# Kernel tuning notes

Hardware: AMD Instinct MI355X
Metric: run time of the kernel (lower is better)

The kernel has to match this reference:

```python
import jax, jax.numpy as jnp
import numpy as np

B, N, M, L, H = 32, 4096, 256, 128, 4
GAMMA = 2.0


def setup_inputs() -> dict:
    key = jax.random.key(0)
    kx, km, kv, ku, kw = jax.random.split(key, 5)
    x = jax.random.normal(kx, (B, N, M), dtype=jnp.float32)
    masks = (jax.random.uniform(km, (B, N)) > 0.3).astype(jnp.float32)
    # VarianceScaling(scale=0.1, fan_in, uniform) ~ small init; exact dist doesn't affect math
    V = jax.random.normal(kv, (H, M, L), dtype=jnp.float32) * 0.02
    U = jax.random.normal(ku, (H, M, L), dtype=jnp.float32) * 0.02
    w = jax.random.normal(kw, (H, L, 1), dtype=jnp.float32) * 0.05
    return {"x": x, "masks": masks, "V": V, "U": U, "w": w}


def reference(x, masks, V, U, w):
    # x: [B,N,M], masks: [B,N], V/U: [H,M,L], w: [H,L,1]
    m = masks[:, None, :, None]  # [B,1,N,1] broadcast over heads
    gated = jnp.tanh(jnp.einsum('bnm,hml->bhnl', x, V)) * jax.nn.sigmoid(
        jnp.einsum('bnm,hml->bhnl', x, U))          # [B,H,N,L]
    logits = jnp.einsum('bhnl,hl->bhn', gated, w[..., 0])[..., None]  # [B,H,N,1]
    a = m * logits                                   # masked logits (as in original)
    a = m * jnp.exp(a)                               # masked exp
    a = a / jnp.sum(a, axis=2, keepdims=True)        # softmax over instances
    ag = a ** GAMMA
    a = ag / jnp.sum(ag, axis=2, keepdims=True)      # gamma-power renorm
    emb = jnp.einsum('bhnk,bnm->bhm', a, x)          # weighted sum; k is the trailing 1
    emb = emb.reshape(B, H * M)                      # concat heads along axis=1
    att = jnp.transpose(a, (1, 0, 2, 3))             # [H,B,N,1] (per-head attention list)
    return (att, emb)
```

## Files before the change

kernel.cpp:

```cpp
#include <hip/hip_runtime.h>
#include <hip/hip_bf16.h>
#include <stdint.h>

#define B_ 32
#define N_ 4096
#define M_ 256
#define L_ 128
#define H_ 4
#define BN_ (B_ * N_)

typedef __bf16 bf16x8 __attribute__((ext_vector_type(8)));
typedef float  f32x4  __attribute__((ext_vector_type(4)));

__device__ __forceinline__ unsigned short f2bf(float f) {
    unsigned int u = __float_as_uint(f);
    u += 0x7fffu + ((u >> 16) & 1u);
    return (unsigned short)(u >> 16);
}
__device__ __forceinline__ unsigned int pack2(float lo, float hi) {
    return (unsigned int)f2bf(lo) | ((unsigned int)f2bf(hi) << 16);
}

__device__ __forceinline__ void gload16(const void* g, void* l) {
    __builtin_amdgcn_global_load_lds(
        (const __attribute__((address_space(1))) unsigned int*)g,
        (__attribute__((address_space(3))) unsigned int*)l, 16, 0, 0);
}


__global__ void prep_x(const float* __restrict__ x, unsigned short* __restrict__ xb) {
    const int blk  = blockIdx.x;
    const int tile = blk >> 2, ks = blk & 3;
    const int i    = threadIdx.x;
    const int kk   = (i & 7) * 8;
    const int tl   = kk >> 5;
    const int kl   = kk & 31;
    char* dst = (char*)xb + ((size_t)tile * 8 + ks * 2 + tl) * 8192;
#pragma unroll
    for (int rep = 0; rep < 4; ++rep) {
        int row = rep * 32 + (i >> 3);
        const float* gx = x + (size_t)(tile * 128 + row) * M_ + ks * 64 + kk;
        float4 a = *(const float4*)gx;
        float4 b = *(const float4*)(gx + 4);
        uint4 o;
        o.x = pack2(a.x, a.y); o.y = pack2(a.z, a.w);
        o.z = pack2(b.x, b.y); o.w = pack2(b.z, b.w);
        int byte = (row * 64 + kl * 2) ^ ((row & 14) << 3);
        *(uint4*)(dst + byte) = o;
    }
}

__global__ void prep_vu_img(const float* __restrict__ V, const float* __restrict__ U,
                            unsigned short* __restrict__ vu) {
    __shared__ float slab[64][129];
    const int b   = blockIdx.x;
    const int mat = b & 1, ks = (b >> 1) & 3, h = b >> 3;
    const float* src = (mat ? U : V) + ((size_t)h * M_ + ks * 64) * L_;
    const int tid = threadIdx.x;
#pragma unroll
    for (int rep = 0; rep < 32; ++rep) {
        int idx = rep * 256 + tid;
        slab[idx >> 7][idx & 127] = src[(size_t)(idx >> 7) * L_ + (idx & 127)];
    }
    __syncthreads();
#pragma unroll
    for (int rep = 0; rep < 4; ++rep) {
        int cidx = rep * 256 + tid;
        int l  = cidx >> 3;
        int kk = (cidx & 7) * 8;
        uint4 o;
        o.x = pack2(slab[kk + 0][l], slab[kk + 1][l]);
        o.y = pack2(slab[kk + 2][l], slab[kk + 3][l]);
        o.z = pack2(slab[kk + 4][l], slab[kk + 5][l]);
        o.w = pack2(slab[kk + 6][l], slab[kk + 7][l]);
        int tl = kk >> 5, kl = kk & 31;
        char* dst = (char*)vu + (((size_t)(h * 8 + ks * 2 + tl)) * 2 + mat) * 8192;
        int byte = (l * 64 + kl * 2) ^ ((l & 14) << 3);
        *(uint4*)(dst + byte) = o;
    }
}

__global__ __launch_bounds__(256, 3)
void gemm_fast6(const unsigned short* __restrict__ xb,
                const unsigned short* __restrict__ vu,
                const float* __restrict__ w,
                float* __restrict__ logits) {
    __shared__ __align__(16) unsigned short xs[2][4096];
    __shared__ __align__(16) unsigned short vs[2][4096];
    __shared__ __align__(16) unsigned short us[2][4096];
    __shared__ float part[2][128];

    const int orig    = blockIdx.x;
    const int logical = (orig & 7) * 512 + (orig >> 3);
    const int tile    = logical >> 2;
    const int h       = logical & 3;

    const int tid  = threadIdx.x;
    const int lane = tid & 63;
    const int wv   = tid >> 6;
    const int g    = lane >> 4;
    const int c    = lane & 15;
    const int wr   = wv & 1;
    const int wc   = wv >> 1;

    f32x4 accV[4][4], accU[4][4];
#pragma unroll
    for (int rf = 0; rf < 4; ++rf)
#pragma unroll
        for (int cf = 0; cf < 4; ++cf) {
            accV[rf][cf] = (f32x4){0.f, 0.f, 0.f, 0.f};
            accU[rf][cf] = (f32x4){0.f, 0.f, 0.f, 0.f};
        }

    const int soff = wv * 2048;

    const char* gxs = (const char*)xb + (size_t)tile * 65536 + soff + lane * 16;
    const char* gvs = (const char*)vu + (size_t)h * 131072 + soff + lane * 16;
    const char* gus = gvs + 8192;

    int aoff[4], boff[4];
#pragma unroll
    for (int rf = 0; rf < 4; ++rf) {
        int r = wr * 64 + rf * 16 + c;
        aoff[rf] = (r * 64 + g * 16) ^ ((r & 14) << 3);
    }
#pragma unroll
    for (int cf = 0; cf < 4; ++cf) {
        int l = wc * 64 + cf * 16 + c;
        boff[cf] = (l * 64 + g * 16) ^ ((l & 14) << 3);
    }

#define SCHED __builtin_amdgcn_sched_barrier(0)

#define STAGE(t, bufi) do {                                          \
        const char* _gx = gxs + (t) * 8192;                          \
        const char* _gv = gvs + (t) * 16384;                         \
        const char* _gu = gus + (t) * 16384;                         \
        gload16(_gx,        (char*)xs[bufi] + soff);                 \
        gload16(_gx + 1024, (char*)xs[bufi] + soff + 1024);          \
        gload16(_gv,        (char*)vs[bufi] + soff);                 \
        gload16(_gv + 1024, (char*)vs[bufi] + soff + 1024);          \
        gload16(_gu,        (char*)us[bufi] + soff);                 \
        gload16(_gu + 1024, (char*)us[bufi] + soff + 1024);          \
    } while (0)

    STAGE(0, 0);
    SCHED;

#pragma unroll
    for (int t = 0; t < 8; ++t) {
        asm volatile("s_waitcnt vmcnt(0)" ::: "memory");
        __builtin_amdgcn_s_barrier();
        SCHED;

        if (t < 7) STAGE(t + 1, (t + 1) & 1);
        SCHED;

        const int buf = t & 1;
        const char* xbuf = (const char*)xs[buf];
        const char* vbuf = (const char*)vs[buf];
        const char* ubuf = (const char*)us[buf];

        bf16x8 a0 = *(const bf16x8*)(xbuf + aoff[0]);
        bf16x8 a1 = *(const bf16x8*)(xbuf + aoff[1]);
        bf16x8 a2 = *(const bf16x8*)(xbuf + aoff[2]);
        bf16x8 a3 = *(const bf16x8*)(xbuf + aoff[3]);
        __builtin_amdgcn_s_setprio(1);
#pragma unroll
        for (int cf = 0; cf < 4; ++cf) {
            bf16x8 bv = *(const bf16x8*)(vbuf + boff[cf]);
            bf16x8 bu = *(const bf16x8*)(ubuf + boff[cf]);
            accV[0][cf] = __builtin_amdgcn_mfma_f32_16x16x32_bf16(a0, bv, accV[0][cf], 0, 0, 0);
            accV[1][cf] = __builtin_amdgcn_mfma_f32_16x16x32_bf16(a1, bv, accV[1][cf], 0, 0, 0);
            accV[2][cf] = __builtin_amdgcn_mfma_f32_16x16x32_bf16(a2, bv, accV[2][cf], 0, 0, 0);
            accV[3][cf] = __builtin_amdgcn_mfma_f32_16x16x32_bf16(a3, bv, accV[3][cf], 0, 0, 0);
            accU[0][cf] = __builtin_amdgcn_mfma_f32_16x16x32_bf16(a0, bu, accU[0][cf], 0, 0, 0);
            accU[1][cf] = __builtin_amdgcn_mfma_f32_16x16x32_bf16(a1, bu, accU[1][cf], 0, 0, 0);
            accU[2][cf] = __builtin_amdgcn_mfma_f32_16x16x32_bf16(a2, bu, accU[2][cf], 0, 0, 0);
            accU[3][cf] = __builtin_amdgcn_mfma_f32_16x16x32_bf16(a3, bu, accU[3][cf], 0, 0, 0);
        }
        __builtin_amdgcn_s_setprio(0);
    }
#undef STAGE
#undef SCHED

    const float* wrow = w + h * L_ + wc * 64;
#pragma unroll
    for (int rf = 0; rf < 4; ++rf) {
        float plog[4] = {0.f, 0.f, 0.f, 0.f};
#pragma unroll
        for (int cf = 0; cf < 4; ++cf) {
            float wvv = wrow[cf * 16 + c];
#pragma unroll
            for (int i = 0; i < 4; ++i) {
                float vv = accV[rf][cf][i];
                float uu = accU[rf][cf][i];
                vv = fminf(fmaxf(vv, -20.f), 20.f);
                float A = __expf(2.f * vv);
                float E = __expf(fminf(-uu, 30.f));
                float gg = __fdividef(A - 1.f, (A + 1.f) * (1.f + E));
                plog[i] += gg * wvv;
            }
        }
#pragma unroll
        for (int i = 0; i < 4; ++i) {
            float v = plog[i];
            v += __shfl_xor(v, 1);
            v += __shfl_xor(v, 2);
            v += __shfl_xor(v, 4);
            v += __shfl_xor(v, 8);
            if (c == 0)
                part[wc][wr * 64 + rf * 16 + g * 4 + i] = v;
        }
    }
    __syncthreads();
    if (tid < 128) {
        float v = part[0][tid] + part[1][tid];
        int rowflat = tile * 128 + tid;
        int b = rowflat >> 12;
        int n = rowflat & (N_ - 1);
        logits[((size_t)b * H_ + h) * N_ + n] = v;
    }
}

__global__ void prep_vu_slow(const float* __restrict__ V, const float* __restrict__ U,
                             unsigned short* __restrict__ Vt, unsigned short* __restrict__ Ut) {
    int idx = blockIdx.x * 256 + threadIdx.x;
    int m = idx & (M_ - 1);
    int l = (idx >> 8) & (L_ - 1);
    int h = idx >> 15;
    Vt[idx] = f2bf(V[((size_t)h * M_ + m) * L_ + l]);
    Ut[idx] = f2bf(U[((size_t)h * M_ + m) * L_ + l]);
}

#define BM 128
#define BK 64

__global__ __launch_bounds__(256, 2)
void gemm_logits(const float* __restrict__ x,
                 const unsigned short* __restrict__ Vt,
                 const unsigned short* __restrict__ Ut,
                 const float* __restrict__ w,
                 float* __restrict__ logits) {
    __shared__ __align__(16) unsigned short xs[BM * BK];
    __shared__ __align__(16) unsigned short vs[L_ * BK];
    __shared__ __align__(16) unsigned short us[L_ * BK];
    __shared__ float wl[L_];

    const int h    = blockIdx.x >> 10;
    const int tile = blockIdx.x & 1023;
    const int row0 = tile * BM;
    const int tid  = threadIdx.x;
    const int lane = tid & 63;
    const int wave = tid >> 6;

    if (tid < L_) wl[tid] = w[h * L_ + tid];

    f32x4 accV[2][8], accU[2][8];
#pragma unroll
    for (int rf = 0; rf < 2; ++rf)
#pragma unroll
        for (int cf = 0; cf < 8; ++cf) {
            accV[rf][cf] = (f32x4){0.f, 0.f, 0.f, 0.f};
            accU[rf][cf] = (f32x4){0.f, 0.f, 0.f, 0.f};
        }

    const unsigned short* Vh = Vt + (size_t)h * L_ * M_;
    const unsigned short* Uh = Ut + (size_t)h * L_ * M_;
    const int g = lane >> 4;
    const int c = lane & 15;

    for (int ks = 0; ks < 4; ++ks) {
        const int k0 = ks * BK;
        __syncthreads();
#pragma unroll
        for (int p = 0; p < 4; ++p) {
            int row = p * 32 + (tid >> 3);
            int kk  = (tid & 7) * 8;
            const float* gx = x + (size_t)(row0 + row) * M_ + k0 + kk;
            float4 a = *(const float4*)gx;
            float4 b = *(const float4*)(gx + 4);
            uint4 o;
            o.x = pack2(a.x, a.y); o.y = pack2(a.z, a.w);
            o.z = pack2(b.x, b.y); o.w = pack2(b.z, b.w);
            int byte = (row * BK + kk) * 2;
            byte ^= (row & 7) << 4;
            *(uint4*)((char*)xs + byte) = o;
        }
#pragma unroll
        for (int p = 0; p < 4; ++p) {
            int l  = p * 32 + (tid >> 3);
            int kk = (tid & 7) * 8;
            uint4 v = *(const uint4*)(Vh + (size_t)l * M_ + k0 + kk);
            uint4 u = *(const uint4*)(Uh + (size_t)l * M_ + k0 + kk);
            int byte = (l * BK + kk) * 2;
            byte ^= (l & 7) << 4;
            *(uint4*)((char*)vs + byte) = v;
            *(uint4*)((char*)us + byte) = u;
        }
        __syncthreads();
#pragma unroll
        for (int ksub = 0; ksub < 2; ++ksub) {
            bf16x8 afr[2];
#pragma unroll
            for (int rf = 0; rf < 2; ++rf) {
                int row = wave * 32 + rf * 16 + c;
                int byte = (row * BK + ksub * 32 + g * 8) * 2;
                byte ^= (row & 7) << 4;
                afr[rf] = *(const bf16x8*)((const char*)xs + byte);
            }
#pragma unroll
            for (int cf = 0; cf < 8; ++cf) {
                int l = cf * 16 + c;
                int byte = (l * BK + ksub * 32 + g * 8) * 2;
                byte ^= (l & 7) << 4;
                bf16x8 bv = *(const bf16x8*)((const char*)vs + byte);
                bf16x8 bu = *(const bf16x8*)((const char*)us + byte);
#pragma unroll
                for (int rf = 0; rf < 2; ++rf) {
                    accV[rf][cf] = __builtin_amdgcn_mfma_f32_16x16x32_bf16(afr[rf], bv, accV[rf][cf], 0, 0, 0);
                    accU[rf][cf] = __builtin_amdgcn_mfma_f32_16x16x32_bf16(afr[rf], bu, accU[rf][cf], 0, 0, 0);
                }
            }
        }
    }
#pragma unroll
    for (int rf = 0; rf < 2; ++rf) {
        float plog[4] = {0.f, 0.f, 0.f, 0.f};
#pragma unroll
        for (int cf = 0; cf < 8; ++cf) {
            float wvv = wl[cf * 16 + c];
#pragma unroll
            for (int i = 0; i < 4; ++i) {
                float vv = accV[rf][cf][i];
                float uu = accU[rf][cf][i];
                vv = fminf(fmaxf(vv, -20.f), 20.f);
                float e2v = __expf(2.f * vv);
                float t = __fdividef(e2v - 1.f, e2v + 1.f);
                float s = __fdividef(1.f, 1.f + __expf(-uu));
                plog[i] += t * s * wvv;
            }
        }
#pragma unroll
        for (int i = 0; i < 4; ++i) {
            float v = plog[i];
            v += __shfl_xor(v, 1);
            v += __shfl_xor(v, 2);
            v += __shfl_xor(v, 4);
            v += __shfl_xor(v, 8);
            if (c == 0) {
                int rowflat = row0 + wave * 32 + rf * 16 + g * 4 + i;
                int b = rowflat >> 12;
                int n = rowflat & (N_ - 1);
                logits[((size_t)b * H_ + h) * N_ + n] = v;
            }
        }
    }
}

__global__ __launch_bounds__(256)
void softmax_att(const float* __restrict__ logits, const float* __restrict__ masks,
                 float* __restrict__ att) {
    const int bh = blockIdx.x;
    const int b = bh >> 2, h = bh & 3;
    __shared__ float e2s[N_];
    __shared__ float red[4];
    const int tid = threadIdx.x;

    float sum = 0.f;
#pragma unroll
    for (int i = 0; i < N_ / 256; ++i) {
        int n = i * 256 + tid;
        float lg = logits[((size_t)b * H_ + h) * N_ + n];
        float mv = masks[(size_t)b * N_ + n];
        float e = mv * __expf(mv * lg);
        float e2 = e * e;
        e2s[n] = e2;
        sum += e2;
    }
#pragma unroll
    for (int off = 32; off >= 1; off >>= 1) sum += __shfl_xor(sum, off);
    if ((tid & 63) == 0) red[tid >> 6] = sum;
    __syncthreads();
    float S = red[0] + red[1] + red[2] + red[3];
    float inv = 1.f / S;
#pragma unroll
    for (int i = 0; i < N_ / 256; ++i) {
        int n = i * 256 + tid;
        att[((size_t)h * B_ + b) * N_ + n] = e2s[n] * inv;
    }
}

#define NCH 32
#define CHUNK (N_ / NCH)

__global__ __launch_bounds__(256)
void emb_partial(const float* __restrict__ x, const float* __restrict__ att,
                 float* __restrict__ part) {
    const int bc = blockIdx.x;
    const int b = bc >> 5, ch = bc & 31;
    __shared__ float as[H_][CHUNK];
    const int tid = threadIdx.x;

    for (int i = tid; i < H_ * CHUNK; i += 256) {
        int hh = i >> 7;
        int j  = i & (CHUNK - 1);
        as[hh][j] = att[((size_t)hh * B_ + b) * N_ + ch * CHUNK + j];
    }
    __syncthreads();

    float a0 = 0.f, a1 = 0.f, a2 = 0.f, a3 = 0.f;
    const float* xp = x + ((size_t)b * N_ + ch * CHUNK) * M_ + tid;
#pragma unroll 4
    for (int j = 0; j < CHUNK; ++j) {
        float xv = xp[(size_t)j * M_];
        a0 += as[0][j] * xv;
        a1 += as[1][j] * xv;
        a2 += as[2][j] * xv;
        a3 += as[3][j] * xv;
    }
    float* pp = part + (size_t)bc * H_ * M_ + tid;
    pp[0 * M_] = a0; pp[1 * M_] = a1; pp[2 * M_] = a2; pp[3 * M_] = a3;
}

__global__ __launch_bounds__(256)
void emb_reduce(const float* __restrict__ part, float* __restrict__ emb) {
    int idx = blockIdx.x * 256 + threadIdx.x;
    int b = idx >> 10;
    int r = idx & 1023;
    float s = 0.f;
#pragma unroll
    for (int ci = 0; ci < NCH; ++ci)
        s += part[((size_t)(b * NCH + ci)) * (H_ * M_) + r];
    emb[idx] = s;
}

extern "C" void kernel_launch(void* const* d_in, const int* in_sizes, int n_in,
                              void* d_out, int out_size, void* d_ws, size_t ws_size,
                              hipStream_t stream) {
    const float* x     = (const float*)d_in[0];
    const float* masks = (const float*)d_in[1];
    const float* V     = (const float*)d_in[2];
    const float* U     = (const float*)d_in[3];
    const float* w     = (const float*)d_in[4];

    float* att = (float*)d_out;
    float* emb = att + (size_t)H_ * B_ * N_;

    char* ws = (char*)d_ws;
    const size_t XB_BYTES  = (size_t)1024 * 8 * 8192;
    const size_t VU_BYTES  = (size_t)64 * 8192;
    const size_t LG_BYTES  = (size_t)B_ * H_ * N_ * 4;
    const size_t PT_BYTES  = (size_t)B_ * NCH * H_ * M_ * 4;
    const size_t NEED_FAST = XB_BYTES + VU_BYTES + LG_BYTES + PT_BYTES;

    float* logits;
    float* partp;

    if (ws_size >= NEED_FAST) {
        unsigned short* xb = (unsigned short*)ws;
        unsigned short* vuimg = (unsigned short*)(ws + XB_BYTES);
        logits = (float*)(ws + XB_BYTES + VU_BYTES);
        partp  = (float*)(ws + XB_BYTES + VU_BYTES + LG_BYTES);

        prep_x     <<<4096, 256, 0, stream>>>(x, xb);
        prep_vu_img<<<32,   256, 0, stream>>>(V, U, vuimg);
        gemm_fast6 <<<4096, 256, 0, stream>>>(xb, vuimg, w, logits);
    } else {
        unsigned short* Vt = (unsigned short*)ws;
        unsigned short* Ut = (unsigned short*)(ws + 262144);
        logits = (float*)(ws + 524288);
        partp  = (float*)(ws + 524288 + LG_BYTES);

        prep_vu_slow<<<512, 256, 0, stream>>>(V, U, Vt, Ut);
        gemm_logits <<<4096, 256, 0, stream>>>(x, Vt, Ut, w, logits);
    }

    softmax_att<<<B_ * H_,              256, 0, stream>>>(logits, masks, att);
    emb_partial<<<B_ * NCH,             256, 0, stream>>>(x, att, partp);
    emb_reduce <<<(B_ * H_ * M_) / 256, 256, 0, stream>>>(partp, emb);
}
```

Before: 174.0 us.

## Fuse fp32-to-bf16 x conversion into GEMM and prescale weights for cheaper gating

Removes the separate prep_x pass, which wrote a bf16 swizzled copy of x to a workspace. The GEMM now loads fp32 x straight into registers, converts it in-kernel and writes it to LDS after the MFMA block, overlapping that work with compute. V is prescaled by 2 and U by -1 so the epilogue can call exp directly, dropping the clamps and multiplies. This saves a full write and re-read of x, but adds VALU conversion and register pressure to the GEMM. Without the clamps, exp can overflow to inf and the tanh expression can become NaN for large activations.

```diff
diff --git a/kernel.cpp b/kernel.cpp
--- a/kernel.cpp
+++ b/kernel.cpp
@@ -28,39 +28,18 @@
 }
 
 
-__global__ void prep_x(const float* __restrict__ x, unsigned short* __restrict__ xb) {
-    const int blk  = blockIdx.x;
-    const int tile = blk >> 2, ks = blk & 3;
-    const int i    = threadIdx.x;
-    const int kk   = (i & 7) * 8;
-    const int tl   = kk >> 5;
-    const int kl   = kk & 31;
-    char* dst = (char*)xb + ((size_t)tile * 8 + ks * 2 + tl) * 8192;
-#pragma unroll
-    for (int rep = 0; rep < 4; ++rep) {
-        int row = rep * 32 + (i >> 3);
-        const float* gx = x + (size_t)(tile * 128 + row) * M_ + ks * 64 + kk;
-        float4 a = *(const float4*)gx;
-        float4 b = *(const float4*)(gx + 4);
-        uint4 o;
-        o.x = pack2(a.x, a.y); o.y = pack2(a.z, a.w);
-        o.z = pack2(b.x, b.y); o.w = pack2(b.z, b.w);
-        int byte = (row * 64 + kl * 2) ^ ((row & 14) << 3);
-        *(uint4*)(dst + byte) = o;
-    }
-}
-
 __global__ void prep_vu_img(const float* __restrict__ V, const float* __restrict__ U,
                             unsigned short* __restrict__ vu) {
     __shared__ float slab[64][129];
     const int b   = blockIdx.x;
     const int mat = b & 1, ks = (b >> 1) & 3, h = b >> 3;
     const float* src = (mat ? U : V) + ((size_t)h * M_ + ks * 64) * L_;
+    const float scale = mat ? -1.0f : 2.0f;
     const int tid = threadIdx.x;
 #pragma unroll
     for (int rep = 0; rep < 32; ++rep) {
         int idx = rep * 256 + tid;
-        slab[idx >> 7][idx & 127] = src[(size_t)(idx >> 7) * L_ + (idx & 127)];
+        slab[idx >> 7][idx & 127] = scale * src[(size_t)(idx >> 7) * L_ + (idx & 127)];
     }
     __syncthreads();
 #pragma unroll
@@ -81,7 +60,7 @@
 }
 
 __global__ __launch_bounds__(256, 3)
-void gemm_fast6(const unsigned short* __restrict__ xb,
+void gemm_fast7(const float* __restrict__ x,
                 const unsigned short* __restrict__ vu,
                 const float* __restrict__ w,
                 float* __restrict__ logits) {
@@ -114,9 +93,15 @@
 
     const int soff = wv * 2048;
 
-    const char* gxs = (const char*)xb + (size_t)tile * 65536 + soff + lane * 16;
     const char* gvs = (const char*)vu + (size_t)h * 131072 + soff + lane * 16;
     const char* gus = gvs + 8192;
+
+    const int rL   = lane >> 1;
+    const int half = lane & 1;
+    const float* gx = x + ((size_t)tile * 128 + wv * 32 + rL) * M_ + half * 16;
+
+    const int xrow = wv * 32 + rL;
+    const int xb0  = (xrow * 64 + half * 32) ^ ((xrow & 14) << 3);
 
     int aoff[4], boff[4];
 #pragma unroll
@@ -130,21 +115,46 @@
         boff[cf] = (l * 64 + g * 16) ^ ((l & 14) << 3);
     }
 
+    float4 xr0, xr1, xr2, xr3;
+
 #define SCHED __builtin_amdgcn_sched_barrier(0)
 
-#define STAGE(t, bufi) do {                                          \
-        const char* _gx = gxs + (t) * 8192;                          \
+#define LOADX(t) do {                                                \
+        xr0 = *(const float4*)(gx + (t) * 32);                       \
+        xr1 = *(const float4*)(gx + (t) * 32 + 4);                   \
+        xr2 = *(const float4*)(gx + (t) * 32 + 8);                   \
+        xr3 = *(const float4*)(gx + (t) * 32 + 12);                  \
+    } while (0)
+
+#define WRITEX(bufi) do {                                            \
+        bf16x8 lo, hi;                                               \
+        lo[0] = (__bf16)xr0.x; lo[1] = (__bf16)xr0.y;                \
+        lo[2] = (__bf16)xr0.z; lo[3] = (__bf16)xr0.w;                \
+        lo[4] = (__bf16)xr1.x; lo[5] = (__bf16)xr1.y;                \
+        lo[6] = (__bf16)xr1.z; lo[7] = (__bf16)xr1.w;                \
+        hi[0] = (__bf16)xr2.x; hi[1] = (__bf16)xr2.y;                \
+        hi[2] = (__bf16)xr2.z; hi[3] = (__bf16)xr2.w;                \
+        hi[4] = (__bf16)xr3.x; hi[5] = (__bf16)xr3.y;                \
+        hi[6] = (__bf16)xr3.z; hi[7] = (__bf16)xr3.w;                \
+        *(bf16x8*)((char*)xs[bufi] + xb0)        = lo;               \
+        *(bf16x8*)((char*)xs[bufi] + (xb0 ^ 16)) = hi;               \
+    } while (0)
+
+#define STAGEB(t, bufi) do {                                         \
         const char* _gv = gvs + (t) * 16384;                         \
         const char* _gu = gus + (t) * 16384;                         \
-        gload16(_gx,        (char*)xs[bufi] + soff);                 \
-        gload16(_gx + 1024, (char*)xs[bufi] + soff + 1024);          \
         gload16(_gv,        (char*)vs[bufi] + soff);                 \
         gload16(_gv + 1024, (char*)vs[bufi] + soff + 1024);          \
         gload16(_gu,        (char*)us[bufi] + soff);                 \
         gload16(_gu + 1024, (char*)us[bufi] + soff + 1024);          \
     } while (0)
 
-    STAGE(0, 0);
+    LOADX(0);
+    SCHED;
+    STAGEB(0, 0);
+    SCHED;
+    WRITEX(0);
+    asm volatile("s_waitcnt lgkmcnt(0)" ::: "memory");
     SCHED;
 
 #pragma unroll
@@ -153,8 +163,12 @@
         __builtin_amdgcn_s_barrier();
         SCHED;
 
-        if (t < 7) STAGE(t + 1, (t + 1) & 1);
-        SCHED;
+        if (t < 7) {
+            LOADX(t + 1);
+            SCHED;
+            STAGEB(t + 1, (t + 1) & 1);
+            SCHED;
+        }
 
         const int buf = t & 1;
         const char* xbuf = (const char*)xs[buf];
@@ -180,8 +194,17 @@
             accU[3][cf] = __builtin_amdgcn_mfma_f32_16x16x32_bf16(a3, bu, accU[3][cf], 0, 0, 0);
         }
         __builtin_amdgcn_s_setprio(0);
-    }
-#undef STAGE
+        SCHED;
+
+        if (t < 7) {
+            WRITEX((t + 1) & 1);
+        }
+        asm volatile("s_waitcnt lgkmcnt(0)" ::: "memory");
+        SCHED;
+    }
+#undef STAGEB
+#undef WRITEX
+#undef LOADX
 #undef SCHED
 
     const float* wrow = w + h * L_ + wc * 64;
@@ -193,11 +216,8 @@
             float wvv = wrow[cf * 16 + c];
 #pragma unroll
             for (int i = 0; i < 4; ++i) {
-                float vv = accV[rf][cf][i];
-                float uu = accU[rf][cf][i];
-                vv = fminf(fmaxf(vv, -20.f), 20.f);
-                float A = __expf(2.f * vv);
-                float E = __expf(fminf(-uu, 30.f));
+                float A = __expf(accV[rf][cf][i]);
+                float E = __expf(accU[rf][cf][i]);
                 float gg = __fdividef(A - 1.f, (A + 1.f) * (1.f + E));
                 plog[i] += gg * wvv;
             }
@@ -448,24 +468,21 @@
     float* emb = att + (size_t)H_ * B_ * N_;
 
     char* ws = (char*)d_ws;
-    const size_t XB_BYTES  = (size_t)1024 * 8 * 8192;
     const size_t VU_BYTES  = (size_t)64 * 8192;
     const size_t LG_BYTES  = (size_t)B_ * H_ * N_ * 4;
     const size_t PT_BYTES  = (size_t)B_ * NCH * H_ * M_ * 4;
-    const size_t NEED_FAST = XB_BYTES + VU_BYTES + LG_BYTES + PT_BYTES;
+    const size_t NEED_FAST = VU_BYTES + LG_BYTES + PT_BYTES;
 
     float* logits;
     float* partp;
 
     if (ws_size >= NEED_FAST) {
-        unsigned short* xb = (unsigned short*)ws;
-        unsigned short* vuimg = (unsigned short*)(ws + XB_BYTES);
-        logits = (float*)(ws + XB_BYTES + VU_BYTES);
-        partp  = (float*)(ws + XB_BYTES + VU_BYTES + LG_BYTES);
-
-        prep_x     <<<4096, 256, 0, stream>>>(x, xb);
+        unsigned short* vuimg = (unsigned short*)ws;
+        logits = (float*)(ws + VU_BYTES);
+        partp  = (float*)(ws + VU_BYTES + LG_BYTES);
+
         prep_vu_img<<<32,   256, 0, stream>>>(V, U, vuimg);
-        gemm_fast6 <<<4096, 256, 0, stream>>>(xb, vuimg, w, logits);
+        gemm_fast7 <<<4096, 256, 0, stream>>>(x, vuimg, w, logits);
     } else {
         unsigned short* Vt = (unsigned short*)ws;
         unsigned short* Ut = (unsigned short*)(ws + 262144);
```

Result: slower. 219.9 us (+26.3%).
